# Kernel optimization log

Hardware: AMD Instinct MI355X
Metric: run time of the kernel (lower is better)

The kernel has to match this reference:

```python
import jax, jax.numpy as jnp
from jax import lax
import numpy as np


def conv4d(x, w, b, pad):
    """4D conv (stride 1) as a sum of 3D convs over the first-spatial-dim kernel taps.
    x: [B, Cin, T, D, H, W]; w: [Cout, Cin, Kt, Kd, Kh, Kw]; same pad on all dims."""
    B, Cin, T, D, H, W = x.shape
    Cout, _, Kt = w.shape[:3]
    xp = jnp.pad(x, ((0, 0), (0, 0), (pad, pad), (0, 0), (0, 0), (0, 0)))
    Tout = T + 2 * pad - Kt + 1
    acc = None
    for k in range(Kt):  # loop over kernel taps (<=3), not data dims
        xs = xp[:, :, k:k + Tout]                      # [B,Cin,Tout,D,H,W]
        xs = xs.transpose(0, 2, 1, 3, 4, 5).reshape(B * Tout, Cin, D, H, W)
        y = lax.conv_general_dilated(
            xs, w[:, :, k], (1, 1, 1), [(pad, pad)] * 3,
            dimension_numbers=('NCDHW', 'OIDHW', 'NCDHW'))
        acc = y if acc is None else acc + y
    Do, Ho, Wo = acc.shape[2:]
    out = acc.reshape(B, Tout, Cout, Do, Ho, Wo).transpose(0, 2, 1, 3, 4, 5)
    return out + b[None, :, None, None, None, None]


def tconv4d_k2s2(x, w, b):
    """4D transposed conv, kernel=2, stride=2, pad=0 (non-overlapping blocks).
    x: [B,Cin,T,D,H,W]; w: [Cin,Cout,2,2,2,2] (PyTorch ConvTranspose layout)."""
    B, Cin, T, D, H, W = x.shape
    Cout = w.shape[1]
    y = jnp.einsum('bcijkl,copqrs->boipjqkrls', x, w)
    y = y.reshape(B, Cout, 2 * T, 2 * D, 2 * H, 2 * W)
    return y + b[None, :, None, None, None, None]


def setup_inputs() -> dict:
    key = jax.random.key(0)
    ks = jax.random.split(key, 10)
    Cin, Cout = 64, 32
    x1 = jax.random.normal(ks[0], (2, Cin, 8, 8, 8, 8), dtype=jnp.float32)
    x2 = jax.random.normal(ks[1], (2, Cin // 2, 16, 16, 16, 16), dtype=jnp.float32)
    def w(k, shape, fan_in):
        return jax.random.normal(k, shape, dtype=jnp.float32) / np.float32(np.sqrt(fan_in))
    up_w = w(ks[2], (Cin, Cin // 2, 2, 2, 2, 2), Cin * 16)
    up_b = w(ks[3], (Cin // 2,), Cin * 16)
    w1 = w(ks[4], (Cout, Cin, 3, 3, 3, 3), Cin * 81)
    b1 = w(ks[5], (Cout,), Cin * 81)
    w2 = w(ks[6], (Cout, Cout, 3, 3, 3, 3), Cout * 81)
    b2 = w(ks[7], (Cout,), Cout * 81)
    w3 = w(ks[8], (Cout, Cin, 1, 1, 1, 1), Cin)
    b3 = w(ks[9], (Cout,), Cin)
    return {'x1': x1, 'x2': x2, 'up_w': up_w, 'up_b': up_b,
            'w1': w1, 'b1': b1, 'w2': w2, 'b2': b2, 'w3': w3, 'b3': b3}


def reference(x1, x2, up_w, up_b, w1, b1, w2, b2, w3, b3):
    x1u = tconv4d_k2s2(x1, up_w, up_b)              # [B, Cin//2, 16,16,16,16]
    xc = jnp.concatenate([x2, x1u], axis=1)          # [B, Cin, 16,16,16,16]
    Y = jax.nn.relu(conv4d(xc, w1, b1, 1))
    Y = conv4d(Y, w2, b2, 1)
    sc = conv4d(xc, w3, b3, 0)                       # 1x1 residual projection
    return jax.nn.relu(Y + sc)
```

## Files before the change

kernel.cpp:

```cpp
#include <hip/hip_runtime.h>

typedef unsigned short u16;
typedef __attribute__((ext_vector_type(8))) short short8;
typedef __attribute__((ext_vector_type(4))) float f32x4;

#define XCB_OFF  0
#define Y1B_OFF  8388608
#define W1P_OFF  12582912
#define W2P_OFF  12748800
#define W3P_OFF  12831744
#define UPWP_OFF 12833792
#define X1T_OFF  12866560

__device__ __forceinline__ u16 f2bf(float v) {
    unsigned u = __builtin_bit_cast(unsigned, v);
    u += 0x7FFFu + ((u >> 16) & 1u);
    return (u16)(u >> 16);
}

__device__ __forceinline__ f32x4 MFMA(short8 a, short8 b, f32x4 c) {
    return __builtin_amdgcn_mfma_f32_16x16x32_bf16(a, b, c, 0, 0, 0);
}

__device__ __forceinline__ void decode_bid(int bid, int& b, int& t, int& d, int& h0) {
    int xcd = bid & 7, loc = bid >> 3;
    int hB = loc & 1;
    d = (loc >> 1) & 15;
    int tsub = (loc >> 5) & 1;
    b = loc >> 6;
    t = xcd * 2 + tsub;
    h0 = hB * 8;
}

__global__ __launch_bounds__(256) void setup(const float* __restrict__ w1,
                                             const float* __restrict__ w2,
                                             const float* __restrict__ w3,
                                             const float* __restrict__ upw,
                                             const float* __restrict__ x1,
                                             const float* __restrict__ x2,
                                             u16* __restrict__ ws) {
    __shared__ u16 lds[256 * 66];
    int bid = blockIdx.x;
    int tid = threadIdx.x;
    if (bid < 1108) {
        int idx = bid * 256 + tid;
        if (idx < 165888) {
            int j = idx & 7, lane = (idx >> 3) & 63, rest = idx >> 9;
            int half = rest & 1, chunk = (rest >> 1) & 1, tap = rest >> 2;
            int co = half * 16 + (lane & 15), ci = chunk * 32 + (lane >> 4) * 8 + j;
            ws[W1P_OFF + idx] = f2bf(w1[(co * 64 + ci) * 81 + tap]);
        } else if (idx < 165888 + 82944) {
            int i2 = idx - 165888;
            int j = i2 & 7, lane = (i2 >> 3) & 63, rest = i2 >> 9;
            int half = rest & 1, tap = rest >> 1;
            int co = half * 16 + (lane & 15), ci = (lane >> 4) * 8 + j;
            ws[W2P_OFF + i2] = f2bf(w2[(co * 32 + ci) * 81 + tap]);
        } else if (idx < 165888 + 82944 + 2048) {
            int i3 = idx - (165888 + 82944);
            int j = i3 & 7, lane = (i3 >> 3) & 63, rest = i3 >> 9;
            int half = rest & 1, chunk = rest >> 1;
            int co = half * 16 + (lane & 15), ci = chunk * 32 + (lane >> 4) * 8 + j;
            ws[W3P_OFF + i3] = f2bf(w3[co * 64 + ci]);
        } else if (idx < 250880 + 32768) {
            int i4 = idx - 250880;
            int j = i4 & 7, lane = (i4 >> 3) & 63, rest = i4 >> 9;
            int half = rest & 1, chunk = (rest >> 1) & 1, tap = rest >> 2;
            int co = half * 16 + (lane & 15), ci = chunk * 32 + (lane >> 4) * 8 + j;
            ws[UPWP_OFF + i4] = f2bf(upw[(ci * 32 + co) * 16 + tap]);
        }
    } else if (bid < 1620) {
        int lb = bid - 1108;
        int b = lb >> 8;
        int pos_base = (lb & 255) * 256;
        u16* xcb = ws + XCB_OFF;
        #pragma unroll
        for (int c = 0; c < 32; ++c) {
            lds[tid * 40 + c] = f2bf(x2[((b * 32 + c) << 16) + pos_base + tid]);
        }
        __syncthreads();
        #pragma unroll
        for (int k = 0; k < 4; ++k) {
            int f = k * 256 + tid;
            int u = f & 3, pos = f >> 2;
            uint4 v = *(const uint4*)(lds + pos * 40 + u * 8);
            *(uint4*)(xcb + (size_t)((b << 16) + pos_base + pos) * 64 + u * 8) = v;
        }
    } else {
        int lb = bid - 1620;
        int b = lb >> 4;
        int pos_base = (lb & 15) * 256;
        u16* x1t = ws + X1T_OFF;
        #pragma unroll
        for (int c = 0; c < 64; ++c) {
            lds[tid * 66 + c] = f2bf(x1[((b * 64 + c) << 12) + pos_base + tid]);
        }
        __syncthreads();
        #pragma unroll
        for (int k = 0; k < 64; ++k) {
            int f = k * 256 + tid;
            int ci = f & 63, pos = f >> 6;
            x1t[(size_t)((b << 12) + pos_base + pos) * 64 + ci] = lds[pos * 66 + ci];
        }
    }
}

__global__ __launch_bounds__(256) void xc_up_mfma(const u16* __restrict__ x1t,
                                                  const u16* __restrict__ upwp,
                                                  const float* __restrict__ up_b,
                                                  u16* __restrict__ xcb) {
    int tid = threadIdx.x;
    int wv = tid >> 6, lane = tid & 63;
    int q = lane >> 4, m = lane & 15;
    int wid = blockIdx.x * 4 + wv;
    int j = wid & 63, tap = (wid >> 6) & 15, b = wid >> 10;

    f32x4 acc[4][2];
    {
        float4 bi0 = ((const float4*)up_b)[q];
        float4 bi1 = ((const float4*)up_b)[4 + q];
        #pragma unroll
        for (int g = 0; g < 4; ++g) {
            acc[g][0] = (f32x4){bi0.x, bi0.y, bi0.z, bi0.w};
            acc[g][1] = (f32x4){bi1.x, bi1.y, bi1.z, bi1.w};
        }
    }

    const short8* wv8 = (const short8*)upwp;
    const u16* xb = x1t + (size_t)((b << 12) + (j << 6) + m) * 64;
    #pragma unroll
    for (int chunk = 0; chunk < 2; ++chunk) {
        short8 a0 = wv8[((tap * 2 + chunk) * 2 + 0) * 64 + lane];
        short8 a1 = wv8[((tap * 2 + chunk) * 2 + 1) * 64 + lane];
        #pragma unroll
        for (int g = 0; g < 4; ++g) {
            short8 bf = *(const short8*)(xb + (size_t)(g * 16) * 64 + chunk * 32 + q * 8);
            acc[g][0] = MFMA(a0, bf, acc[g][0]);
            acc[g][1] = MFMA(a1, bf, acc[g][1]);
        }
    }

    int it = j >> 3, id = j & 7;
    int pt = tap >> 3, pd = (tap >> 2) & 1, ph = (tap >> 1) & 1, pw = tap & 1;
    int oT = 2 * it + pt, oD = 2 * id + pd, oW = 2 * (m & 7) + pw;
    #pragma unroll
    for (int g = 0; g < 4; ++g) {
        int ih = g * 2 + (m >> 3);
        int opos = oT * 4096 + oD * 256 + (2 * ih + ph) * 16 + oW;
        u16* op = xcb + (size_t)((b << 16) + opos) * 64 + 32 + q * 4;
        #pragma unroll
        for (int half = 0; half < 2; ++half) {
            f32x4 v = acc[g][half];
            uint2 o;
            o.x = (unsigned)f2bf(v.x) | ((unsigned)f2bf(v.y) << 16);
            o.y = (unsigned)f2bf(v.z) | ((unsigned)f2bf(v.w) << 16);
            *(uint2*)(op + half * 16) = o;
        }
    }
}

__global__ __launch_bounds__(256) void conv1_mfma(const u16* __restrict__ xcb,
                                                  const u16* __restrict__ w1p,
                                                  const float* __restrict__ b1,
                                                  u16* __restrict__ y1b) {
    __shared__ u16 lds[11520];
    int tid = threadIdx.x;
    int lane = tid & 63, wv = tid >> 6;
    int q = lane >> 4, m = lane & 15;
    int c = wv & 1, rg = wv >> 1;
    int b, t, d, h0;
    decode_bid(blockIdx.x, b, t, d, h0);

    f32x4 acc[4][2];
    if (c == 0) {
        float4 bi0 = ((const float4*)b1)[q];
        float4 bi1 = ((const float4*)b1)[4 + q];
        #pragma unroll
        for (int i = 0; i < 4; ++i) {
            acc[i][0] = (f32x4){bi0.x, bi0.y, bi0.z, bi0.w};
            acc[i][1] = (f32x4){bi1.x, bi1.y, bi1.z, bi1.w};
        }
    } else {
        #pragma unroll
        for (int i = 0; i < 4; ++i) {
            acc[i][0] = (f32x4){0.f, 0.f, 0.f, 0.f};
            acc[i][1] = (f32x4){0.f, 0.f, 0.f, 0.f};
        }
    }
    const short8* w1v = (const short8*)w1p;

    for (int ktd = 0; ktd < 9; ++ktd) {
        int kt = ktd / 3, kd = ktd - kt * 3;
        int tt = t + kt - 1, dd = d + kd - 1;
        bool pv = ((unsigned)tt < 16u) && ((unsigned)dd < 16u);
        __syncthreads();
        int pbase = ((b * 16 + tt) * 16 + dd) * 256;
        for (int ui = tid; ui < 1440; ui += 256) {
            int u = ui & 7, p = (ui >> 3) % 18, hh = ui / 144;
            int gh = h0 - 1 + hh, gw = p - 1;
            uint4 val = {0, 0, 0, 0};
            if (pv && (unsigned)gh < 16u && (unsigned)gw < 16u) {
                val = *(const uint4*)(xcb + (size_t)(pbase + gh * 16 + gw) * 64 + u * 8);
            }
            *(uint4*)(lds + hh * 1152 + p * 64 + ((u ^ (p & 7)) * 8)) = val;
        }
        __syncthreads();
        #pragma unroll
        for (int kw = 0; kw < 3; ++kw) {
            int p = kw + m, pm = p & 7;
            int bo = p * 64 + ((((c << 2) | q) ^ pm) << 3);
            short8 R[6];
            #pragma unroll
            for (int r = 0; r < 6; ++r) {
                R[r] = *(const short8*)(lds + (rg * 4 + r) * 1152 + bo);
            }
            #pragma unroll
            for (int kh = 0; kh < 3; ++kh) {
                int tap = (ktd * 3 + kh) * 3 + kw;
                short8 a0 = w1v[((tap * 2 + c) * 2 + 0) * 64 + lane];
                short8 a1 = w1v[((tap * 2 + c) * 2 + 1) * 64 + lane];
                #pragma unroll
                for (int i = 0; i < 4; ++i) {
                    acc[i][0] = MFMA(a0, R[i + kh], acc[i][0]);
                    acc[i][1] = MFMA(a1, R[i + kh], acc[i][1]);
                }
            }
        }
    }

    __syncthreads();
    f32x4* buf = (f32x4*)lds;
    if (c == 1) {
        #pragma unroll
        for (int i = 0; i < 4; ++i)
            #pragma unroll
            for (int half = 0; half < 2; ++half)
                buf[((rg * 4 + i) * 2 + half) * 64 + lane] = acc[i][half];
    }
    __syncthreads();
    if (c == 0) {
        int obase = ((b * 16 + t) * 16 + d) * 256 + (h0 + rg * 4) * 16 + m;
        #pragma unroll
        for (int i = 0; i < 4; ++i) {
            int pos = obase + i * 16;
            #pragma unroll
            for (int half = 0; half < 2; ++half) {
                f32x4 v = acc[i][half];
                f32x4 w = buf[((rg * 4 + i) * 2 + half) * 64 + lane];
                v.x += w.x; v.y += w.y; v.z += w.z; v.w += w.w;
                unsigned r0 = f2bf(fmaxf(v.x, 0.f)), r1 = f2bf(fmaxf(v.y, 0.f));
                unsigned r2 = f2bf(fmaxf(v.z, 0.f)), r3 = f2bf(fmaxf(v.w, 0.f));
                uint2 o;
                o.x = r0 | (r1 << 16);
                o.y = r2 | (r3 << 16);
                *(uint2*)(y1b + (size_t)pos * 32 + half * 16 + q * 4) = o;
            }
        }
    }
}

__global__ __launch_bounds__(256) void conv2_mfma(const u16* __restrict__ y1b,
                                                  const u16* __restrict__ xcb,
                                                  const u16* __restrict__ w2p,
                                                  const u16* __restrict__ w3p,
                                                  const float* __restrict__ b2,
                                                  const float* __restrict__ b3,
                                                  float* __restrict__ out) {
    __shared__ u16 lds[5760];
    int tid = threadIdx.x;
    int lane = tid & 63, wv = tid >> 6;
    int q = lane >> 4, m = lane & 15;
    int hf = wv & 1, rg = wv >> 1;
    int b, t, d, h0;
    decode_bid(blockIdx.x, b, t, d, h0);

    f32x4 acc[4];
    {
        float4 p0 = ((const float4*)b2)[hf * 4 + q];
        float4 s0 = ((const float4*)b3)[hf * 4 + q];
        #pragma unroll
        for (int i = 0; i < 4; ++i)
            acc[i] = (f32x4){p0.x + s0.x, p0.y + s0.y, p0.z + s0.z, p0.w + s0.w};
    }
    const short8* w2v = (const short8*)w2p;

    for (int ktd = 0; ktd < 9; ++ktd) {
        int kt = ktd / 3, kd = ktd - kt * 3;
        int tt = t + kt - 1, dd = d + kd - 1;
        bool pv = ((unsigned)tt < 16u) && ((unsigned)dd < 16u);
        __syncthreads();
        int pbase = ((b * 16 + tt) * 16 + dd) * 256;
        for (int ui = tid; ui < 720; ui += 256) {
            int u = ui & 3, p = (ui >> 2) % 18, hh = ui / 72;
            int gh = h0 - 1 + hh, gw = p - 1;
            uint4 val = {0, 0, 0, 0};
            if (pv && (unsigned)gh < 16u && (unsigned)gw < 16u) {
                val = *(const uint4*)(y1b + (size_t)(pbase + gh * 16 + gw) * 32 + u * 8);
            }
            *(uint4*)(lds + hh * 576 + p * 32 + ((u ^ (p & 3)) * 8)) = val;
        }
        __syncthreads();
        #pragma unroll
        for (int kw = 0; kw < 3; ++kw) {
            int p = kw + m, pm = p & 3;
            int bo = p * 32 + ((q ^ pm) << 3);
            short8 R[6];
            #pragma unroll
            for (int r = 0; r < 6; ++r) {
                R[r] = *(const short8*)(lds + (rg * 4 + r) * 576 + bo);
            }
            #pragma unroll
            for (int kh = 0; kh < 3; ++kh) {
                int tap = (ktd * 3 + kh) * 3 + kw;
                short8 a = w2v[(tap * 2 + hf) * 64 + lane];
                #pragma unroll
                for (int i = 0; i < 4; ++i) {
                    acc[i] = MFMA(a, R[i + kh], acc[i]);
                }
            }
        }
    }

    const short8* w3v = (const short8*)w3p;
    int lpos0 = (t * 16 + d) * 256 + (h0 + rg * 4) * 16 + m;
    int gpos0 = (b << 16) + lpos0;
    #pragma unroll
    for (int chunk = 0; chunk < 2; ++chunk) {
        short8 a = w3v[(chunk * 2 + hf) * 64 + lane];
        #pragma unroll
        for (int i = 0; i < 4; ++i) {
            short8 bf = *(const short8*)(xcb + (size_t)(gpos0 + i * 16) * 64 + ((chunk << 2) | q) * 8);
            acc[i] = MFMA(a, bf, acc[i]);
        }
    }

    #pragma unroll
    for (int i = 0; i < 4; ++i) {
        int lpos = lpos0 + i * 16;
        f32x4 v = acc[i];
        int co = hf * 16 + q * 4;
        float* op = out + (((size_t)(b * 32 + co)) << 16) + lpos;
        op[0ull << 16] = fmaxf(v.x, 0.f);
        op[1ull << 16] = fmaxf(v.y, 0.f);
        op[2ull << 16] = fmaxf(v.z, 0.f);
        op[3ull << 16] = fmaxf(v.w, 0.f);
    }
}

extern "C" void kernel_launch(void* const* d_in, const int* in_sizes, int n_in,
                              void* d_out, int out_size, void* d_ws, size_t ws_size,
                              hipStream_t stream) {
    const float* x1   = (const float*)d_in[0];
    const float* x2   = (const float*)d_in[1];
    const float* up_w = (const float*)d_in[2];
    const float* up_b = (const float*)d_in[3];
    const float* w1   = (const float*)d_in[4];
    const float* b1   = (const float*)d_in[5];
    const float* w2   = (const float*)d_in[6];
    const float* b2   = (const float*)d_in[7];
    const float* w3   = (const float*)d_in[8];
    const float* b3   = (const float*)d_in[9];
    u16* ws  = (u16*)d_ws;
    float* out = (float*)d_out;

    setup<<<1652, 256, 0, stream>>>(w1, w2, w3, up_w, x1, x2, ws);
    xc_up_mfma<<<512, 256, 0, stream>>>(ws + X1T_OFF, ws + UPWP_OFF, up_b, ws + XCB_OFF);
    conv1_mfma<<<1024, 256, 0, stream>>>(ws + XCB_OFF, ws + W1P_OFF, b1, ws + Y1B_OFF);
    conv2_mfma<<<1024, 256, 0, stream>>>(ws + Y1B_OFF, ws + XCB_OFF, ws + W2P_OFF,
                                         ws + W3P_OFF, b2, b3, out);
}
```

Baseline: 170.7 us.

## Register-prefetch next input plane in conv1/conv2 and precompute staging offsets

Both conv kernels now load the next (kt,kd) input plane from global memory into registers while the current plane is consumed from LDS. This overlaps global-load latency with MFMA work. Per-thread LDS and global offsets and bounds masks are computed once, outside the loop. Launch bounds request 4 blocks per CU, which caps register use and risks spills given the extra prefetch registers.

```diff
diff --git a/kernel.cpp b/kernel.cpp
--- a/kernel.cpp
+++ b/kernel.cpp
@@ -158,10 +158,10 @@
     }
 }
 
-__global__ __launch_bounds__(256) void conv1_mfma(const u16* __restrict__ xcb,
-                                                  const u16* __restrict__ w1p,
-                                                  const float* __restrict__ b1,
-                                                  u16* __restrict__ y1b) {
+__global__ __launch_bounds__(256, 4) void conv1_mfma(const u16* __restrict__ xcb,
+                                                     const u16* __restrict__ w1p,
+                                                     const float* __restrict__ b1,
+                                                     u16* __restrict__ y1b) {
     __shared__ u16 lds[11520];
     int tid = threadIdx.x;
     int lane = tid & 63, wv = tid >> 6;
@@ -170,6 +170,19 @@
     int b, t, d, h0;
     decode_bid(blockIdx.x, b, t, d, h0);
 
+    int lofs[6], gofs[6];
+    bool st[6], inr[6];
+    #pragma unroll
+    for (int k = 0; k < 6; ++k) {
+        int ui = tid + k * 256;
+        int u = ui & 7, p = (ui >> 3) % 18, hh = ui / 144;
+        int gh = h0 - 1 + hh, gw = p - 1;
+        st[k] = ui < 1440;
+        inr[k] = st[k] && ((unsigned)gh < 16u) && ((unsigned)gw < 16u);
+        gofs[k] = (gh * 16 + gw) * 64 + u * 8;
+        lofs[k] = hh * 1152 + p * 64 + ((u ^ (p & 7)) * 8);
+    }
+
     f32x4 acc[4][2];
     if (c == 0) {
         float4 bi0 = ((const float4*)b1)[q];
@@ -188,21 +201,30 @@
     }
     const short8* w1v = (const short8*)w1p;
 
-    for (int ktd = 0; ktd < 9; ++ktd) {
+    uint4 rP[6];
+    auto load_plane = [&](int ktd) {
         int kt = ktd / 3, kd = ktd - kt * 3;
         int tt = t + kt - 1, dd = d + kd - 1;
         bool pv = ((unsigned)tt < 16u) && ((unsigned)dd < 16u);
-        __syncthreads();
-        int pbase = ((b * 16 + tt) * 16 + dd) * 256;
-        for (int ui = tid; ui < 1440; ui += 256) {
-            int u = ui & 7, p = (ui >> 3) % 18, hh = ui / 144;
-            int gh = h0 - 1 + hh, gw = p - 1;
-            uint4 val = {0, 0, 0, 0};
-            if (pv && (unsigned)gh < 16u && (unsigned)gw < 16u) {
-                val = *(const uint4*)(xcb + (size_t)(pbase + gh * 16 + gw) * 64 + u * 8);
-            }
-            *(uint4*)(lds + hh * 1152 + p * 64 + ((u ^ (p & 7)) * 8)) = val;
-        }
+        const u16* src = xcb + (size_t)(size_t)(((b * 16 + tt) * 16 + dd)) * 16384;
+        #pragma unroll
+        for (int k = 0; k < 6; ++k) {
+            uint4 v = {0, 0, 0, 0};
+            if (pv && inr[k]) v = *(const uint4*)(src + gofs[k]);
+            rP[k] = v;
+        }
+    };
+    auto write_plane = [&]() {
+        #pragma unroll
+        for (int k = 0; k < 6; ++k)
+            if (st[k]) *(uint4*)(lds + lofs[k]) = rP[k];
+    };
+
+    load_plane(0);
+    for (int ktd = 0; ktd < 9; ++ktd) {
+        __syncthreads();
+        write_plane();
+        if (ktd < 8) load_plane(ktd + 1);
         __syncthreads();
         #pragma unroll
         for (int kw = 0; kw < 3; ++kw) {
@@ -210,9 +232,8 @@
             int bo = p * 64 + ((((c << 2) | q) ^ pm) << 3);
             short8 R[6];
             #pragma unroll
-            for (int r = 0; r < 6; ++r) {
+            for (int r = 0; r < 6; ++r)
                 R[r] = *(const short8*)(lds + (rg * 4 + r) * 1152 + bo);
-            }
             #pragma unroll
             for (int kh = 0; kh < 3; ++kh) {
                 int tap = (ktd * 3 + kh) * 3 + kw;
@@ -258,13 +279,13 @@
     }
 }
 
-__global__ __launch_bounds__(256) void conv2_mfma(const u16* __restrict__ y1b,
-                                                  const u16* __restrict__ xcb,
-                                                  const u16* __restrict__ w2p,
-                                                  const u16* __restrict__ w3p,
-                                                  const float* __restrict__ b2,
-                                                  const float* __restrict__ b3,
-                                                  float* __restrict__ out) {
+__global__ __launch_bounds__(256, 4) void conv2_mfma(const u16* __restrict__ y1b,
+                                                     const u16* __restrict__ xcb,
+                                                     const u16* __restrict__ w2p,
+                                                     const u16* __restrict__ w3p,
+                                                     const float* __restrict__ b2,
+                                                     const float* __restrict__ b3,
+                                                     float* __restrict__ out) {
     __shared__ u16 lds[5760];
     int tid = threadIdx.x;
     int lane = tid & 63, wv = tid >> 6;
@@ -273,6 +294,19 @@
     int b, t, d, h0;
     decode_bid(blockIdx.x, b, t, d, h0);
 
+    int lofs[3], gofs[3];
+    bool st[3], inr[3];
+    #pragma unroll
+    for (int k = 0; k < 3; ++k) {
+        int ui = tid + k * 256;
+        int u = ui & 3, p = (ui >> 2) % 18, hh = ui / 72;
+        int gh = h0 - 1 + hh, gw = p - 1;
+        st[k] = ui < 720;
+        inr[k] = st[k] && ((unsigned)gh < 16u) && ((unsigned)gw < 16u);
+        gofs[k] = (gh * 16 + gw) * 32 + u * 8;
+        lofs[k] = hh * 576 + p * 32 + ((u ^ (p & 3)) * 8);
+    }
+
     f32x4 acc[4];
     {
         float4 p0 = ((const float4*)b2)[hf * 4 + q];
@@ -283,21 +317,30 @@
     }
     const short8* w2v = (const short8*)w2p;
 
-    for (int ktd = 0; ktd < 9; ++ktd) {
+    uint4 rP[3];
+    auto load_plane = [&](int ktd) {
         int kt = ktd / 3, kd = ktd - kt * 3;
         int tt = t + kt - 1, dd = d + kd - 1;
         bool pv = ((unsigned)tt < 16u) && ((unsigned)dd < 16u);
-        __syncthreads();
-        int pbase = ((b * 16 + tt) * 16 + dd) * 256;
-        for (int ui = tid; ui < 720; ui += 256) {
-            int u = ui & 3, p = (ui >> 2) % 18, hh = ui / 72;
-            int gh = h0 - 1 + hh, gw = p - 1;
-            uint4 val = {0, 0, 0, 0};
-            if (pv && (unsigned)gh < 16u && (unsigned)gw < 16u) {
-                val = *(const uint4*)(y1b + (size_t)(pbase + gh * 16 + gw) * 32 + u * 8);
-            }
-            *(uint4*)(lds + hh * 576 + p * 32 + ((u ^ (p & 3)) * 8)) = val;
-        }
+        const u16* src = y1b + (size_t)(size_t)(((b * 16 + tt) * 16 + dd)) * 8192;
+        #pragma unroll
+        for (int k = 0; k < 3; ++k) {
+            uint4 v = {0, 0, 0, 0};
+            if (pv && inr[k]) v = *(const uint4*)(src + gofs[k]);
+            rP[k] = v;
+        }
+    };
+    auto write_plane = [&]() {
+        #pragma unroll
+        for (int k = 0; k < 3; ++k)
+            if (st[k]) *(uint4*)(lds + lofs[k]) = rP[k];
+    };
+
+    load_plane(0);
+    for (int ktd = 0; ktd < 9; ++ktd) {
+        __syncthreads();
+        write_plane();
+        if (ktd < 8) load_plane(ktd + 1);
         __syncthreads();
         #pragma unroll
         for (int kw = 0; kw < 3; ++kw) {
@@ -305,9 +348,8 @@
             int bo = p * 32 + ((q ^ pm) << 3);
             short8 R[6];
             #pragma unroll
-            for (int r = 0; r < 6; ++r) {
+            for (int r = 0; r < 6; ++r)
                 R[r] = *(const short8*)(lds + (rg * 4 + r) * 576 + bo);
-            }
             #pragma unroll
             for (int kh = 0; kh < 3; ++kh) {
                 int tap = (ktd * 3 + kh) * 3 + kw;
```

After: 169.3 us. No clear change (-0.8%).

## Load conv input operands directly from global memory instead of LDS staging

Applied to the files above, without the earlier changes.

Both conv kernels drop the per-tap LDS staging loop and its two barriers, and each wave now loads its MFMA B operands straight from global memory with bounds masks. Taps whose t/d index falls in the padding are skipped entirely. Launch bounds now request 4 blocks per SIMD-group to raise occupancy. The cost is more global/L2 traffic from redundant loads across waves, and the loads are no longer shared through LDS.

```diff
diff --git a/kernel.cpp b/kernel.cpp
--- a/kernel.cpp
+++ b/kernel.cpp
@@ -158,17 +158,19 @@
     }
 }
 
-__global__ __launch_bounds__(256) void conv1_mfma(const u16* __restrict__ xcb,
-                                                  const u16* __restrict__ w1p,
-                                                  const float* __restrict__ b1,
-                                                  u16* __restrict__ y1b) {
-    __shared__ u16 lds[11520];
+__global__ __launch_bounds__(256, 4) void conv1_mfma(const u16* __restrict__ xcb,
+                                                     const u16* __restrict__ w1p,
+                                                     const float* __restrict__ b1,
+                                                     u16* __restrict__ y1b) {
+    __shared__ f32x4 red[1024];
     int tid = threadIdx.x;
     int lane = tid & 63, wv = tid >> 6;
     int q = lane >> 4, m = lane & 15;
     int c = wv & 1, rg = wv >> 1;
     int b, t, d, h0;
     decode_bid(blockIdx.x, b, t, d, h0);
+    int hbase = h0 + rg * 4 - 1;
+    int coff = ((c << 2) | q) * 8;
 
     f32x4 acc[4][2];
     if (c == 0) {
@@ -191,27 +193,21 @@
     for (int ktd = 0; ktd < 9; ++ktd) {
         int kt = ktd / 3, kd = ktd - kt * 3;
         int tt = t + kt - 1, dd = d + kd - 1;
-        bool pv = ((unsigned)tt < 16u) && ((unsigned)dd < 16u);
-        __syncthreads();
-        int pbase = ((b * 16 + tt) * 16 + dd) * 256;
-        for (int ui = tid; ui < 1440; ui += 256) {
-            int u = ui & 7, p = (ui >> 3) % 18, hh = ui / 144;
-            int gh = h0 - 1 + hh, gw = p - 1;
-            uint4 val = {0, 0, 0, 0};
-            if (pv && (unsigned)gh < 16u && (unsigned)gw < 16u) {
-                val = *(const uint4*)(xcb + (size_t)(pbase + gh * 16 + gw) * 64 + u * 8);
-            }
-            *(uint4*)(lds + hh * 1152 + p * 64 + ((u ^ (p & 7)) * 8)) = val;
-        }
-        __syncthreads();
+        if (((unsigned)tt >= 16u) || ((unsigned)dd >= 16u)) continue;
+        const u16* pb = xcb + (size_t)((b * 16 + tt) * 16 + dd) * 16384;
         #pragma unroll
         for (int kw = 0; kw < 3; ++kw) {
-            int p = kw + m, pm = p & 7;
-            int bo = p * 64 + ((((c << 2) | q) ^ pm) << 3);
+            int gw = kw - 1 + m;
+            bool vw = (unsigned)gw < 16u;
+            int lo = gw * 64 + coff;
             short8 R[6];
             #pragma unroll
             for (int r = 0; r < 6; ++r) {
-                R[r] = *(const short8*)(lds + (rg * 4 + r) * 1152 + bo);
+                int gh = hbase + r;
+                short8 v = {0, 0, 0, 0, 0, 0, 0, 0};
+                if (vw && (unsigned)gh < 16u)
+                    v = *(const short8*)(pb + gh * 1024 + lo);
+                R[r] = v;
             }
             #pragma unroll
             for (int kh = 0; kh < 3; ++kh) {
@@ -227,14 +223,12 @@
         }
     }
 
-    __syncthreads();
-    f32x4* buf = (f32x4*)lds;
     if (c == 1) {
         #pragma unroll
         for (int i = 0; i < 4; ++i)
             #pragma unroll
             for (int half = 0; half < 2; ++half)
-                buf[((rg * 4 + i) * 2 + half) * 64 + lane] = acc[i][half];
+                red[((rg * 4 + i) * 2 + half) * 64 + lane] = acc[i][half];
     }
     __syncthreads();
     if (c == 0) {
@@ -245,7 +239,7 @@
             #pragma unroll
             for (int half = 0; half < 2; ++half) {
                 f32x4 v = acc[i][half];
-                f32x4 w = buf[((rg * 4 + i) * 2 + half) * 64 + lane];
+                f32x4 w = red[((rg * 4 + i) * 2 + half) * 64 + lane];
                 v.x += w.x; v.y += w.y; v.z += w.z; v.w += w.w;
                 unsigned r0 = f2bf(fmaxf(v.x, 0.f)), r1 = f2bf(fmaxf(v.y, 0.f));
                 unsigned r2 = f2bf(fmaxf(v.z, 0.f)), r3 = f2bf(fmaxf(v.w, 0.f));
@@ -258,20 +252,20 @@
     }
 }
 
-__global__ __launch_bounds__(256) void conv2_mfma(const u16* __restrict__ y1b,
-                                                  const u16* __restrict__ xcb,
-                                                  const u16* __restrict__ w2p,
-                                                  const u16* __restrict__ w3p,
-                                                  const float* __restrict__ b2,
-                                                  const float* __restrict__ b3,
-                                                  float* __restrict__ out) {
-    __shared__ u16 lds[5760];
+__global__ __launch_bounds__(256, 4) void conv2_mfma(const u16* __restrict__ y1b,
+                                                     const u16* __restrict__ xcb,
+                                                     const u16* __restrict__ w2p,
+                                                     const u16* __restrict__ w3p,
+                                                     const float* __restrict__ b2,
+                                                     const float* __restrict__ b3,
+                                                     float* __restrict__ out) {
     int tid = threadIdx.x;
     int lane = tid & 63, wv = tid >> 6;
     int q = lane >> 4, m = lane & 15;
     int hf = wv & 1, rg = wv >> 1;
     int b, t, d, h0;
     decode_bid(blockIdx.x, b, t, d, h0);
+    int hbase = h0 + rg * 4 - 1;
 
     f32x4 acc[4];
     {
@@ -286,27 +280,21 @@
     for (int ktd = 0; ktd < 9; ++ktd) {
         int kt = ktd / 3, kd = ktd - kt * 3;
         int tt = t + kt - 1, dd = d + kd - 1;
-        bool pv = ((unsigned)tt < 16u) && ((unsigned)dd < 16u);
-        __syncthreads();
-        int pbase = ((b * 16 + tt) * 16 + dd) * 256;
-        for (int ui = tid; ui < 720; ui += 256) {
-            int u = ui & 3, p = (ui >> 2) % 18, hh = ui / 72;
-            int gh = h0 - 1 + hh, gw = p - 1;
-            uint4 val = {0, 0, 0, 0};
-            if (pv && (unsigned)gh < 16u && (unsigned)gw < 16u) {
-                val = *(const uint4*)(y1b + (size_t)(pbase + gh * 16 + gw) * 32 + u * 8);
-            }
-            *(uint4*)(lds + hh * 576 + p * 32 + ((u ^ (p & 3)) * 8)) = val;
-        }
-        __syncthreads();
+        if (((unsigned)tt >= 16u) || ((unsigned)dd >= 16u)) continue;
+        const u16* pb = y1b + (size_t)((b * 16 + tt) * 16 + dd) * 8192;
         #pragma unroll
         for (int kw = 0; kw < 3; ++kw) {
-            int p = kw + m, pm = p & 3;
-            int bo = p * 32 + ((q ^ pm) << 3);
+            int gw = kw - 1 + m;
+            bool vw = (unsigned)gw < 16u;
+            int lo = gw * 32 + q * 8;
             short8 R[6];
             #pragma unroll
             for (int r = 0; r < 6; ++r) {
-                R[r] = *(const short8*)(lds + (rg * 4 + r) * 576 + bo);
+                int gh = hbase + r;
+                short8 v = {0, 0, 0, 0, 0, 0, 0, 0};
+                if (vw && (unsigned)gh < 16u)
+                    v = *(const short8*)(pb + gh * 512 + lo);
+                R[r] = v;
             }
             #pragma unroll
             for (int kh = 0; kh < 3; ++kh) {
```

Result: slower. 232.5 us (+36.2%).
